# Optimization experiments

Measured on AMD Instinct MI355X. Metric: run time of the kernel, lower is better.

Reference implementation:

```python
import jax, jax.numpy as jnp
import numpy as np

# config constants (from pose_config)
GROUPS = [[0, 1, 2, 3, 4], [5, 6, 7, 8, 9, 10], [11, 12, 13, 14, 15, 16]]
NORM_SCALE = 1.0
OUT_H, OUT_W = 16, 8


def setup_inputs() -> dict:
    key = jax.random.key(0)
    x = jax.random.normal(key, (2048, 17, 64, 32), dtype=jnp.float32)
    return {"x": x}


def reference(x):
    n, c, _, _ = x.shape
    # bilinear, align_corners=False (half-pixel centers) == jax.image.resize 'linear'
    x = jax.image.resize(x, (n, c, OUT_H, OUT_W), method='linear')
    h, w = OUT_H, OUT_W

    x_flat = x.reshape(n, c, h * w)
    idx = jnp.argmax(x_flat, axis=2)                      # [n, c]
    max_response = jnp.max(x_flat, axis=2)                # [n, c]
    max_index = jnp.stack(
        [(idx % w).astype(jnp.float32), (idx // w).astype(jnp.float32)],
        axis=-1)                                          # [n, c, 2]

    # group-wise reduce (group_mode='sum'): sum heatmaps, mean of max responses
    heatmap = jnp.concatenate(
        [jnp.sum(x[:, g], axis=1, keepdims=True) for g in GROUPS], axis=1)   # [n, G, h, w]
    max_response_2 = jnp.concatenate(
        [jnp.mean(max_response[:, g], axis=1, keepdims=True) for g in GROUPS],
        axis=1)                                           # [n, G]

    # normalize: softmax over spatial dim
    g = heatmap.shape[1]
    heatmap = jax.nn.softmax(
        NORM_SCALE * heatmap.reshape(n, g, h * w), axis=2).reshape(n, g, h, w)

    return heatmap, max_response_2, max_index
```

## Files before the change

### kernel.cpp

```cpp
#include <hip/hip_runtime.h>
#include <math.h>

#define N_CH 17
#define IN_H 64
#define IN_W 32
#define OUT_H 16
#define OUT_W 8
#define HW (OUT_H * OUT_W)
#define S_IN_STRIDE 33
#define S_TMP_STRIDE 33

__device__ __forceinline__ void get_weights(int o, int out_n, int in_n,
                                            float* w, int* s) {
    if (o == 0) {
        *s = 0;
        w[0] = 5.f/28.f; w[1] = 7.f/28.f; w[2] = 7.f/28.f; w[3] = 5.f/28.f;
        w[4] = 3.f/28.f; w[5] = 1.f/28.f; w[6] = 0.f;      w[7] = 0.f;
    } else if (o == out_n - 1) {
        *s = in_n - 8;
        w[0] = 0.f;      w[1] = 0.f;      w[2] = 1.f/28.f; w[3] = 3.f/28.f;
        w[4] = 5.f/28.f; w[5] = 7.f/28.f; w[6] = 7.f/28.f; w[7] = 5.f/28.f;
    } else {
        *s = 4 * o - 2;
        w[0] = 1.f/32.f; w[1] = 3.f/32.f; w[2] = 5.f/32.f; w[3] = 7.f/32.f;
        w[4] = 7.f/32.f; w[5] = 5.f/32.f; w[6] = 3.f/32.f; w[7] = 1.f/32.f;
    }
}

__global__ __launch_bounds__(256)
void heatmap_kernel(const float* __restrict__ x,
                    float* __restrict__ out_heat,
                    float* __restrict__ out_mr,
                    float* __restrict__ out_mi) {
    const int n = blockIdx.x;
    const int t = threadIdx.x;

    __shared__ float s_in[IN_H * S_IN_STRIDE];
    __shared__ float s_tmp[OUT_H * S_TMP_STRIDE];
    __shared__ float s_red[HW];
    __shared__ float s_chmax[N_CH];
    __shared__ float s_bcast;

    float wA[8], wB[8], wC[8];
    int sA, sB, sC = 0;
    get_weights(t >> 5, OUT_H, IN_H, wA, &sA);
    get_weights(8 + (t >> 5), OUT_H, IN_H, wB, &sB);
    if (t < HW) get_weights(t & 7, OUT_W, IN_W, wC, &sC);

    const float* xn = x + (size_t)n * N_CH * IN_H * IN_W;

    float gs0 = 0.f, gs1 = 0.f, gs2 = 0.f;

    float4 la = ((const float4*)xn)[t];
    float4 lb = ((const float4*)xn)[t + 256];

    for (int c = 0; c < N_CH; ++c) {
        {
            int i0 = 4 * t;
            float* p = &s_in[(i0 >> 5) * S_IN_STRIDE + (i0 & 31)];
            p[0] = la.x; p[1] = la.y; p[2] = la.z; p[3] = la.w;
            int i1 = 4 * (t + 256);
            p = &s_in[(i1 >> 5) * S_IN_STRIDE + (i1 & 31)];
            p[0] = lb.x; p[1] = lb.y; p[2] = lb.z; p[3] = lb.w;
        }
        __syncthreads();

        if (c + 1 < N_CH) {
            const float4* src = (const float4*)(xn + (size_t)(c + 1) * IN_H * IN_W);
            la = src[t];
            lb = src[t + 256];
        }

        {
            int col = t & 31;
            float acc = 0.f, acc2 = 0.f;
#pragma unroll
            for (int d = 0; d < 8; ++d)
                acc += wA[d] * s_in[(sA + d) * S_IN_STRIDE + col];
#pragma unroll
            for (int d = 0; d < 8; ++d)
                acc2 += wB[d] * s_in[(sB + d) * S_IN_STRIDE + col];
            s_tmp[(t >> 5) * S_TMP_STRIDE + col] = acc;
            s_tmp[(8 + (t >> 5)) * S_TMP_STRIDE + col] = acc2;
        }
        __syncthreads();

        if (t < HW) {
            int orow = t >> 3;
            float acc = 0.f;
#pragma unroll
            for (int d = 0; d < 8; ++d)
                acc += wC[d] * s_tmp[orow * S_TMP_STRIDE + sC + d];
            s_red[t] = acc;
            if (c < 5)       gs0 += acc;
            else if (c < 11) gs1 += acc;
            else             gs2 += acc;
        }
        __syncthreads();

        if (t < 64) {
            float v0 = s_red[t], v1 = s_red[t + 64];
            float bv; int bi;
            if (v1 > v0) { bv = v1; bi = t + 64; } else { bv = v0; bi = t; }
#pragma unroll
            for (int off = 32; off >= 1; off >>= 1) {
                float ov = __shfl_down(bv, off);
                int   oi = __shfl_down(bi, off);
                if (ov > bv || (ov == bv && oi < bi)) { bv = ov; bi = oi; }
            }
            if (t == 0) {
                s_chmax[c] = bv;
                float* mi = out_mi + ((size_t)n * N_CH + c) * 2;
                mi[0] = (float)(bi & 7);
                mi[1] = (float)(bi >> 3);
            }
        }
        __syncthreads();
    }

    if (t < 3) {
        int lo = (t == 0) ? 0 : ((t == 1) ? 5 : 11);
        int hi = (t == 0) ? 5 : ((t == 1) ? 11 : 17);
        float acc = 0.f;
        for (int c = lo; c < hi; ++c) acc += s_chmax[c];
        out_mr[(size_t)n * 3 + t] = acc / (float)(hi - lo);
    }

    float gsv[3] = {gs0, gs1, gs2};
#pragma unroll 1
    for (int g = 0; g < 3; ++g) {
        if (t < HW) s_red[t] = gsv[g];
        __syncthreads();
        if (t < 64) {
            float bv = fmaxf(s_red[t], s_red[t + 64]);
#pragma unroll
            for (int off = 32; off >= 1; off >>= 1)
                bv = fmaxf(bv, __shfl_down(bv, off));
            if (t == 0) s_bcast = bv;
        }
        __syncthreads();
        float m = s_bcast;
        float e = 0.f;
        if (t < HW) { e = expf(gsv[g] - m); s_red[t] = e; }
        __syncthreads();
        if (t < 64) {
            float sv = s_red[t] + s_red[t + 64];
#pragma unroll
            for (int off = 32; off >= 1; off >>= 1)
                sv += __shfl_down(sv, off);
            if (t == 0) s_bcast = sv;
        }
        __syncthreads();
        if (t < HW)
            out_heat[((size_t)n * 3 + g) * HW + t] = e / s_bcast;
        __syncthreads();
    }
}

extern "C" void kernel_launch(void* const* d_in, const int* in_sizes, int n_in,
                              void* d_out, int out_size, void* d_ws, size_t ws_size,
                              hipStream_t stream) {
    const float* x = (const float*)d_in[0];
    float* out = (float*)d_out;
    const int N = in_sizes[0] / (N_CH * IN_H * IN_W);
    float* out_heat = out;
    float* out_mr   = out_heat + (size_t)N * 3 * HW;
    float* out_mi   = out_mr + (size_t)N * 3;
    heatmap_kernel<<<dim3(N), dim3(256), 0, stream>>>(x, out_heat, out_mr, out_mi);
}
```

Before: 382.7 us.

## Process channels per wavefront independently to remove block barriers in resize loop

Each of the four wavefronts now handles its own channels (c = w, w+4, ...) with a private shared-memory staging buffer, padded with zero borders so edge weights become a uniform symmetric filter times a scale factor. The per-channel __syncthreads barriers are gone, and registers double-buffer 8 float4 loads per lane to prefetch the next channel. Group sums are combined across wavefronts through shared memory at the end. This trades higher register and shared-memory use per block, which may lower occupancy, for less synchronisation and more overlap of loads with compute.

```diff
diff --git a/kernel.cpp b/kernel.cpp
--- a/kernel.cpp
+++ b/kernel.cpp
@@ -6,26 +6,14 @@
 #define IN_W 32
 #define OUT_H 16
 #define OUT_W 8
-#define HW (OUT_H * OUT_W)
-#define S_IN_STRIDE 33
-#define S_TMP_STRIDE 33
-
-__device__ __forceinline__ void get_weights(int o, int out_n, int in_n,
-                                            float* w, int* s) {
-    if (o == 0) {
-        *s = 0;
-        w[0] = 5.f/28.f; w[1] = 7.f/28.f; w[2] = 7.f/28.f; w[3] = 5.f/28.f;
-        w[4] = 3.f/28.f; w[5] = 1.f/28.f; w[6] = 0.f;      w[7] = 0.f;
-    } else if (o == out_n - 1) {
-        *s = in_n - 8;
-        w[0] = 0.f;      w[1] = 0.f;      w[2] = 1.f/28.f; w[3] = 3.f/28.f;
-        w[4] = 5.f/28.f; w[5] = 7.f/28.f; w[6] = 7.f/28.f; w[7] = 5.f/28.f;
-    } else {
-        *s = 4 * o - 2;
-        w[0] = 1.f/32.f; w[1] = 3.f/32.f; w[2] = 5.f/32.f; w[3] = 7.f/32.f;
-        w[4] = 7.f/32.f; w[5] = 5.f/32.f; w[6] = 3.f/32.f; w[7] = 1.f/32.f;
-    }
-}
+#define HW 128
+
+#define SIN_FLOATS (68 * 32)
+#define TMP_STRIDE 37
+#define TMP_FLOATS (16 * TMP_STRIDE)
+#define WAVE_FLOATS (SIN_FLOATS + TMP_FLOATS)
+
+#define EDGE_SCALE (32.f / 28.f)
 
 __global__ __launch_bounds__(256)
 void heatmap_kernel(const float* __restrict__ x,
@@ -34,89 +22,124 @@
                     float* __restrict__ out_mi) {
     const int n = blockIdx.x;
     const int t = threadIdx.x;
-
-    __shared__ float s_in[IN_H * S_IN_STRIDE];
-    __shared__ float s_tmp[OUT_H * S_TMP_STRIDE];
+    const int w = t >> 6;
+    const int l = t & 63;
+
+    __shared__ float s_wave[4 * WAVE_FLOATS];
+    __shared__ float s_comb[12 * HW];
     __shared__ float s_red[HW];
     __shared__ float s_chmax[N_CH];
     __shared__ float s_bcast;
 
-    float wA[8], wB[8], wC[8];
-    int sA, sB, sC = 0;
-    get_weights(t >> 5, OUT_H, IN_H, wA, &sA);
-    get_weights(8 + (t >> 5), OUT_H, IN_H, wB, &sB);
-    if (t < HW) get_weights(t & 7, OUT_W, IN_W, wC, &sC);
-
+    float* sw   = s_wave + w * WAVE_FLOATS;
+    float* stmp = sw + SIN_FLOATS;
+
+    sw[l] = 0.f;
+    sw[2112 + l] = 0.f;
+    {
+        int r = l >> 2, cc = l & 3;
+        int col = (cc < 2) ? cc : (cc + 32);
+        stmp[r * TMP_STRIDE + col] = 0.f;
+    }
+
+    const float W0 = 1.f/32.f, W1 = 3.f/32.f, W2 = 5.f/32.f, W3 = 7.f/32.f;
     const float* xn = x + (size_t)n * N_CH * IN_H * IN_W;
-
-    float gs0 = 0.f, gs1 = 0.f, gs2 = 0.f;
-
-    float4 la = ((const float4*)xn)[t];
-    float4 lb = ((const float4*)xn)[t + 256];
-
-    for (int c = 0; c < N_CH; ++c) {
+    const int col = l & 31;
+    const int rhalf = l >> 5;
+
+    float gl0 = 0.f, gl1 = 0.f, gl2 = 0.f;
+    float gh0 = 0.f, gh1 = 0.f, gh2 = 0.f;
+
+    float4 bufA[8], bufB[8];
+    {
+        const float4* src = (const float4*)(xn + (size_t)w * IN_H * IN_W);
+#pragma unroll
+        for (int j = 0; j < 8; ++j) bufA[j] = src[l + 64 * j];
+    }
+
+    auto process = [&](float4 (&cur)[8], float4 (&nxt)[8], int c, bool pre) {
+        float4* dst = (float4*)(sw + 64);
+#pragma unroll
+        for (int j = 0; j < 8; ++j) dst[l + 64 * j] = cur[j];
+
+        if (pre) {
+            const float4* src = (const float4*)(xn + (size_t)(c + 4) * IN_H * IN_W);
+#pragma unroll
+            for (int j = 0; j < 8; ++j) nxt[j] = src[l + 64 * j];
+        }
+
+        __asm__ __volatile__("" ::: "memory");
+
+        float o[8];
+#pragma unroll
+        for (int k = 0; k < 8; ++k) {
+            int r = rhalf * 8 + k;
+            const float* b = sw + (4 * r) * 32 + col;
+            float acc = W0 * b[0]   + W1 * b[32]  + W2 * b[64]  + W3 * b[96]
+                      + W3 * b[128] + W2 * b[160] + W1 * b[192] + W0 * b[224];
+            if ((k == 0 && rhalf == 0) || (k == 7 && rhalf == 1)) acc *= EDGE_SCALE;
+            o[k] = acc;
+        }
+        __asm__ __volatile__("" ::: "memory");
+#pragma unroll
+        for (int k = 0; k < 8; ++k) {
+            int r = rhalf * 8 + k;
+            stmp[r * TMP_STRIDE + 2 + col] = o[k];
+        }
+        __asm__ __volatile__("" ::: "memory");
+
+        float out0, out1;
         {
-            int i0 = 4 * t;
-            float* p = &s_in[(i0 >> 5) * S_IN_STRIDE + (i0 & 31)];
-            p[0] = la.x; p[1] = la.y; p[2] = la.z; p[3] = la.w;
-            int i1 = 4 * (t + 256);
-            p = &s_in[(i1 >> 5) * S_IN_STRIDE + (i1 & 31)];
-            p[0] = lb.x; p[1] = lb.y; p[2] = lb.z; p[3] = lb.w;
-        }
-        __syncthreads();
-
-        if (c + 1 < N_CH) {
-            const float4* src = (const float4*)(xn + (size_t)(c + 1) * IN_H * IN_W);
-            la = src[t];
-            lb = src[t + 256];
+            int r0 = l >> 3, oc = l & 7;
+            const float* b0 = stmp + r0 * TMP_STRIDE + 4 * oc;
+            out0 = W0*b0[0] + W1*b0[1] + W2*b0[2] + W3*b0[3]
+                 + W3*b0[4] + W2*b0[5] + W1*b0[6] + W0*b0[7];
+            const float* b1 = b0 + 8 * TMP_STRIDE;
+            out1 = W0*b1[0] + W1*b1[1] + W2*b1[2] + W3*b1[3]
+                 + W3*b1[4] + W2*b1[5] + W1*b1[6] + W0*b1[7];
+            float cs = (oc == 0 || oc == 7) ? EDGE_SCALE : 1.f;
+            out0 *= cs; out1 *= cs;
         }
 
         {
-            int col = t & 31;
-            float acc = 0.f, acc2 = 0.f;
-#pragma unroll
-            for (int d = 0; d < 8; ++d)
-                acc += wA[d] * s_in[(sA + d) * S_IN_STRIDE + col];
-#pragma unroll
-            for (int d = 0; d < 8; ++d)
-                acc2 += wB[d] * s_in[(sB + d) * S_IN_STRIDE + col];
-            s_tmp[(t >> 5) * S_TMP_STRIDE + col] = acc;
-            s_tmp[(8 + (t >> 5)) * S_TMP_STRIDE + col] = acc2;
-        }
-        __syncthreads();
-
-        if (t < HW) {
-            int orow = t >> 3;
-            float acc = 0.f;
-#pragma unroll
-            for (int d = 0; d < 8; ++d)
-                acc += wC[d] * s_tmp[orow * S_TMP_STRIDE + sC + d];
-            s_red[t] = acc;
-            if (c < 5)       gs0 += acc;
-            else if (c < 11) gs1 += acc;
-            else             gs2 += acc;
-        }
-        __syncthreads();
-
-        if (t < 64) {
-            float v0 = s_red[t], v1 = s_red[t + 64];
             float bv; int bi;
-            if (v1 > v0) { bv = v1; bi = t + 64; } else { bv = v0; bi = t; }
+            if (out1 > out0) { bv = out1; bi = l + 64; } else { bv = out0; bi = l; }
 #pragma unroll
             for (int off = 32; off >= 1; off >>= 1) {
                 float ov = __shfl_down(bv, off);
                 int   oi = __shfl_down(bi, off);
                 if (ov > bv || (ov == bv && oi < bi)) { bv = ov; bi = oi; }
             }
-            if (t == 0) {
+            if (l == 0) {
                 s_chmax[c] = bv;
                 float* mi = out_mi + ((size_t)n * N_CH + c) * 2;
                 mi[0] = (float)(bi & 7);
                 mi[1] = (float)(bi >> 3);
             }
         }
-        __syncthreads();
-    }
+
+        int g = (c < 5) ? 0 : ((c < 11) ? 1 : 2);
+        if (g == 0)      { gl0 += out0; gh0 += out1; }
+        else if (g == 1) { gl1 += out0; gh1 += out1; }
+        else             { gl2 += out0; gh2 += out1; }
+    };
+
+#pragma unroll
+    for (int i = 0; i < 5; ++i) {
+        int c = w + 4 * i;
+        if (c >= N_CH) break;
+        bool pre = (c + 4) < N_CH;
+        if (i & 1) process(bufB, bufA, c, pre);
+        else       process(bufA, bufB, c, pre);
+    }
+
+    s_comb[(w * 3 + 0) * HW + l]      = gl0;
+    s_comb[(w * 3 + 0) * HW + l + 64] = gh0;
+    s_comb[(w * 3 + 1) * HW + l]      = gl1;
+    s_comb[(w * 3 + 1) * HW + l + 64] = gh1;
+    s_comb[(w * 3 + 2) * HW + l]      = gl2;
+    s_comb[(w * 3 + 2) * HW + l + 64] = gh2;
+    __syncthreads();
 
     if (t < 3) {
         int lo = (t == 0) ? 0 : ((t == 1) ? 5 : 11);
@@ -126,7 +149,14 @@
         out_mr[(size_t)n * 3 + t] = acc / (float)(hi - lo);
     }
 
-    float gsv[3] = {gs0, gs1, gs2};
+    float gsv[3] = {0.f, 0.f, 0.f};
+    if (t < HW) {
+#pragma unroll
+        for (int g = 0; g < 3; ++g)
+            gsv[g] = s_comb[(0 * 3 + g) * HW + t] + s_comb[(1 * 3 + g) * HW + t]
+                   + s_comb[(2 * 3 + g) * HW + t] + s_comb[(3 * 3 + g) * HW + t];
+    }
+
 #pragma unroll 1
     for (int g = 0; g < 3; ++g) {
         if (t < HW) s_red[t] = gsv[g];
```

Result: slower. 422.4 us (+10.4%).

## Process two channels concurrently per block with padded smem and uniform bilinear weights

Applied to the files above, without the earlier changes.

Splits the 256-thread block into two halves that each resize a different channel, so all threads do useful work instead of half idling during the horizontal pass and reductions. Zero-padded shared buffers let every output use the same symmetric 8-tap kernel, with an edge rescale factor in place of per-position weight tables. Global loads are double-buffered across iterations and the barriers are custom lgkmcnt waits. The final softmax, argmax merge and group means run in parallel across separate waves. It raises register and shared memory use, adds a redundant ninth iteration for the odd channel, and sets an occupancy hint of 6 blocks per CU.

```diff
diff --git a/kernel.cpp b/kernel.cpp
--- a/kernel.cpp
+++ b/kernel.cpp
@@ -4,156 +4,163 @@
 #define N_CH 17
 #define IN_H 64
 #define IN_W 32
-#define OUT_H 16
-#define OUT_W 8
-#define HW (OUT_H * OUT_W)
-#define S_IN_STRIDE 33
-#define S_TMP_STRIDE 33
+#define HW 128
 
-__device__ __forceinline__ void get_weights(int o, int out_n, int in_n,
-                                            float* w, int* s) {
-    if (o == 0) {
-        *s = 0;
-        w[0] = 5.f/28.f; w[1] = 7.f/28.f; w[2] = 7.f/28.f; w[3] = 5.f/28.f;
-        w[4] = 3.f/28.f; w[5] = 1.f/28.f; w[6] = 0.f;      w[7] = 0.f;
-    } else if (o == out_n - 1) {
-        *s = in_n - 8;
-        w[0] = 0.f;      w[1] = 0.f;      w[2] = 1.f/28.f; w[3] = 3.f/28.f;
-        w[4] = 5.f/28.f; w[5] = 7.f/28.f; w[6] = 7.f/28.f; w[7] = 5.f/28.f;
-    } else {
-        *s = 4 * o - 2;
-        w[0] = 1.f/32.f; w[1] = 3.f/32.f; w[2] = 5.f/32.f; w[3] = 7.f/32.f;
-        w[4] = 7.f/32.f; w[5] = 5.f/32.f; w[6] = 3.f/32.f; w[7] = 1.f/32.f;
-    }
-}
+#define SIN_CH 2176
+#define TMP_STRIDE 37
+#define TMP_CH (16 * TMP_STRIDE)
+#define EDGE (32.f / 28.f)
 
-__global__ __launch_bounds__(256)
+#define BAR_LGKM() asm volatile("s_waitcnt lgkmcnt(0)\n\ts_barrier" ::: "memory")
+
+__global__ __launch_bounds__(256, 6)
 void heatmap_kernel(const float* __restrict__ x,
                     float* __restrict__ out_heat,
                     float* __restrict__ out_mr,
                     float* __restrict__ out_mi) {
     const int n = blockIdx.x;
     const int t = threadIdx.x;
+    const int w = t >> 6, l = t & 63;
+    const int half = t >> 7;
+    const int tl = t & 127;
+    const int col = tl & 31, q = tl >> 5;
+    const int p = tl;
+    const int r2 = p >> 3, oc = p & 7;
+    const int hpos = w & 1;
 
-    __shared__ float s_in[IN_H * S_IN_STRIDE];
-    __shared__ float s_tmp[OUT_H * S_TMP_STRIDE];
-    __shared__ float s_red[HW];
-    __shared__ float s_chmax[N_CH];
-    __shared__ float s_bcast;
+    __shared__ float s_in[2 * SIN_CH];
+    __shared__ float s_tmp[2 * TMP_CH];
+    __shared__ float s_cval[N_CH * 2];
+    __shared__ int   s_cidx[N_CH * 2];
 
-    float wA[8], wB[8], wC[8];
-    int sA, sB, sC = 0;
-    get_weights(t >> 5, OUT_H, IN_H, wA, &sA);
-    get_weights(8 + (t >> 5), OUT_H, IN_H, wB, &sB);
-    if (t < HW) get_weights(t & 7, OUT_W, IN_W, wC, &sC);
+    float* sw = s_in + half * SIN_CH;
+    float* st = s_tmp + half * TMP_CH;
+
+    s_in[half * SIN_CH + (tl < 64 ? tl : 2048 + tl)] = 0.f;
+    if (t < 128) {
+        int ch = t >> 6, rr = (t >> 2) & 15, jj = t & 3;
+        int cc = (jj < 2) ? jj : jj + 32;
+        s_tmp[ch * TMP_CH + rr * TMP_STRIDE + cc] = 0.f;
+    }
 
     const float* xn = x + (size_t)n * N_CH * IN_H * IN_W;
+    float ga0 = 0.f, ga1 = 0.f, ga2 = 0.f;
 
-    float gs0 = 0.f, gs1 = 0.f, gs2 = 0.f;
+    float4 bA[4], bB[4];
+    {
+        const float4* src = (const float4*)(xn + (size_t)half * (IN_H * IN_W));
+#pragma unroll
+        for (int j = 0; j < 4; ++j) bA[j] = src[tl + 128 * j];
+    }
 
-    float4 la = ((const float4*)xn)[t];
-    float4 lb = ((const float4*)xn)[t + 256];
+    auto process = [&](float4 (&cur)[4], float4 (&nxt)[4], int i) {
+        const int c = 2 * i + half;
+        const bool valid = (c < N_CH);
 
-    for (int c = 0; c < N_CH; ++c) {
-        {
-            int i0 = 4 * t;
-            float* p = &s_in[(i0 >> 5) * S_IN_STRIDE + (i0 & 31)];
-            p[0] = la.x; p[1] = la.y; p[2] = la.z; p[3] = la.w;
-            int i1 = 4 * (t + 256);
-            p = &s_in[(i1 >> 5) * S_IN_STRIDE + (i1 & 31)];
-            p[0] = lb.x; p[1] = lb.y; p[2] = lb.z; p[3] = lb.w;
-        }
-        __syncthreads();
+        float4* dst = (float4*)(sw + 64);
+#pragma unroll
+        for (int j = 0; j < 4; ++j) dst[tl + 128 * j] = cur[j];
 
-        if (c + 1 < N_CH) {
-            const float4* src = (const float4*)(xn + (size_t)(c + 1) * IN_H * IN_W);
-            la = src[t];
-            lb = src[t + 256];
+        if (i < 8) {
+            int cn = 2 * (i + 1) + half;
+            cn = cn > 16 ? 16 : cn;
+            const float4* src = (const float4*)(xn + (size_t)cn * (IN_H * IN_W));
+#pragma unroll
+            for (int j = 0; j < 4; ++j) nxt[j] = src[tl + 128 * j];
         }
 
-        {
-            int col = t & 31;
-            float acc = 0.f, acc2 = 0.f;
+        BAR_LGKM();
+
+        const float W[8] = {1.f/32.f, 3.f/32.f, 5.f/32.f, 7.f/32.f,
+                            7.f/32.f, 5.f/32.f, 3.f/32.f, 1.f/32.f};
+        float v[20];
 #pragma unroll
-            for (int d = 0; d < 8; ++d)
-                acc += wA[d] * s_in[(sA + d) * S_IN_STRIDE + col];
+        for (int d = 0; d < 20; ++d) v[d] = sw[(16 * q + d) * 32 + col];
+
+        BAR_LGKM();
+
+        float o4[4];
 #pragma unroll
-            for (int d = 0; d < 8; ++d)
-                acc2 += wB[d] * s_in[(sB + d) * S_IN_STRIDE + col];
-            s_tmp[(t >> 5) * S_TMP_STRIDE + col] = acc;
-            s_tmp[(8 + (t >> 5)) * S_TMP_STRIDE + col] = acc2;
-        }
-        __syncthreads();
-
-        if (t < HW) {
-            int orow = t >> 3;
+        for (int k = 0; k < 4; ++k) {
             float acc = 0.f;
 #pragma unroll
-            for (int d = 0; d < 8; ++d)
-                acc += wC[d] * s_tmp[orow * S_TMP_STRIDE + sC + d];
-            s_red[t] = acc;
-            if (c < 5)       gs0 += acc;
-            else if (c < 11) gs1 += acc;
-            else             gs2 += acc;
+            for (int d = 0; d < 8; ++d) acc += W[d] * v[4 * k + d];
+            if ((q == 0 && k == 0) || (q == 3 && k == 3)) acc *= EDGE;
+            o4[k] = acc;
         }
-        __syncthreads();
+#pragma unroll
+        for (int k = 0; k < 4; ++k)
+            st[(4 * q + k) * TMP_STRIDE + 2 + col] = o4[k];
 
-        if (t < 64) {
-            float v0 = s_red[t], v1 = s_red[t + 64];
-            float bv; int bi;
-            if (v1 > v0) { bv = v1; bi = t + 64; } else { bv = v0; bi = t; }
+        asm volatile("" ::: "memory");
+
+        float o = 0.f;
+#pragma unroll
+        for (int d = 0; d < 8; ++d) o += W[d] * st[r2 * TMP_STRIDE + 4 * oc + d];
+        if (oc == 0 || oc == 7) o *= EDGE;
+
+        if (valid) {
+            if (c < 5)       ga0 += o;
+            else if (c < 11) ga1 += o;
+            else             ga2 += o;
+
+            float bv = o; int bi = p;
 #pragma unroll
             for (int off = 32; off >= 1; off >>= 1) {
                 float ov = __shfl_down(bv, off);
                 int   oi = __shfl_down(bi, off);
                 if (ov > bv || (ov == bv && oi < bi)) { bv = ov; bi = oi; }
             }
-            if (t == 0) {
-                s_chmax[c] = bv;
-                float* mi = out_mi + ((size_t)n * N_CH + c) * 2;
-                mi[0] = (float)(bi & 7);
-                mi[1] = (float)(bi >> 3);
-            }
+            if (l == 0) { s_cval[2 * c + hpos] = bv; s_cidx[2 * c + hpos] = bi; }
         }
-        __syncthreads();
+    };
+
+#pragma unroll
+    for (int i = 0; i < 9; ++i) {
+        if (i & 1) process(bB, bA, i);
+        else       process(bA, bB, i);
     }
 
-    if (t < 3) {
-        int lo = (t == 0) ? 0 : ((t == 1) ? 5 : 11);
-        int hi = (t == 0) ? 5 : ((t == 1) ? 11 : 17);
-        float acc = 0.f;
-        for (int c = lo; c < hi; ++c) acc += s_chmax[c];
-        out_mr[(size_t)n * 3 + t] = acc / (float)(hi - lo);
-    }
+    __syncthreads();
+    float* s_part = s_in;
+    s_part[(half * 3 + 0) * HW + p] = ga0;
+    s_part[(half * 3 + 1) * HW + p] = ga1;
+    s_part[(half * 3 + 2) * HW + p] = ga2;
+    __syncthreads();
 
-    float gsv[3] = {gs0, gs1, gs2};
-#pragma unroll 1
-    for (int g = 0; g < 3; ++g) {
-        if (t < HW) s_red[t] = gsv[g];
-        __syncthreads();
-        if (t < 64) {
-            float bv = fmaxf(s_red[t], s_red[t + 64]);
+    if (w < 3) {
+        const int g = w;
+        float v0 = s_part[g * HW + l]      + s_part[(3 + g) * HW + l];
+        float v1 = s_part[g * HW + 64 + l] + s_part[(3 + g) * HW + 64 + l];
+        float m = fmaxf(v0, v1);
 #pragma unroll
-            for (int off = 32; off >= 1; off >>= 1)
-                bv = fmaxf(bv, __shfl_down(bv, off));
-            if (t == 0) s_bcast = bv;
+        for (int off = 1; off < 64; off <<= 1) m = fmaxf(m, __shfl_xor(m, off));
+        float e0 = expf(v0 - m), e1 = expf(v1 - m);
+        float s = e0 + e1;
+#pragma unroll
+        for (int off = 1; off < 64; off <<= 1) s += __shfl_xor(s, off);
+        float inv = 1.f / s;
+        float* dsto = out_heat + ((size_t)n * 3 + g) * HW;
+        dsto[l]      = e0 * inv;
+        dsto[l + 64] = e1 * inv;
+    } else {
+        if (l < N_CH) {
+            int c = l;
+            float v0 = s_cval[2 * c], v1 = s_cval[2 * c + 1];
+            int i0 = s_cidx[2 * c], i1 = s_cidx[2 * c + 1];
+            int bi = (v1 > v0) ? i1 : i0;
+            float* mi = out_mi + ((size_t)n * N_CH + c) * 2;
+            mi[0] = (float)(bi & 7);
+            mi[1] = (float)(bi >> 3);
         }
-        __syncthreads();
-        float m = s_bcast;
-        float e = 0.f;
-        if (t < HW) { e = expf(gsv[g] - m); s_red[t] = e; }
-        __syncthreads();
-        if (t < 64) {
-            float sv = s_red[t] + s_red[t + 64];
-#pragma unroll
-            for (int off = 32; off >= 1; off >>= 1)
-                sv += __shfl_down(sv, off);
-            if (t == 0) s_bcast = sv;
+        if (l < 3) {
+            int lo = (l == 0) ? 0 : ((l == 1) ? 5 : 11);
+            int hi = (l == 0) ? 5 : ((l == 1) ? 11 : 17);
+            float acc = 0.f;
+            for (int c2 = lo; c2 < hi; ++c2)
+                acc += fmaxf(s_cval[2 * c2], s_cval[2 * c2 + 1]);
+            out_mr[(size_t)n * 3 + l] = acc / (float)(hi - lo);
         }
-        __syncthreads();
-        if (t < HW)
-            out_heat[((size_t)n * 3 + g) * HW + t] = e / s_bcast;
-        __syncthreads();
     }
 }
 
```

Result: slower. 507.6 us (+32.6%).
